# Kernel tuning notes

Measured on AMD Instinct MI355X. Metric: run time of the kernel, lower is better.

The kernel has to match this reference:

```python
import jax, jax.numpy as jnp
import numpy as np

TWO_PI = 2.0 * np.pi


def _fftfreq(n, d):
    # numpy-compatible fftfreq, trace/grad-safe in d: [0..n/2-1, -n/2..-1]/(n*d)
    k = jnp.arange(n)
    k = jnp.where(k < (n + 1) // 2, k, k - n).astype(jnp.float32)
    return k / (n * d)


def _forward(x, wp1_re, wp1_im, wp2_re, wp2_im, wr_re, wr_im, ty, tx):
    wp1 = (wp1_re + 1j * wp1_im).astype(jnp.complex64)   # [Ci,Co,m1]
    wp2 = (wp2_re + 1j * wp2_im).astype(jnp.complex64)   # [Ci,Co,m2]
    wr = (wr_re + 1j * wr_im).astype(jnp.complex64)      # [Ci,Co,m1,m2]
    Ny, Nx = x.shape[-2], x.shape[-1]
    dty = ty[1] - ty[0]
    dtx = tx[1] - tx[0]

    alpha = jnp.fft.fft2(x, axes=(-2, -1))               # [B,Ci,Ny,Nx] complex
    lam1 = (1j * TWO_PI * _fftfreq(Ny, dty)).astype(jnp.complex64)  # [Ny]
    lam2 = (1j * TWO_PI * _fftfreq(Nx, dtx)).astype(jnp.complex64)  # [Nx]

    # Pole-residue transfer function factors: Hw = wr / ((lam1-p1)(lam2-p2))
    A1 = 1.0 / (lam1 - wp1[..., None])                   # [Ci,Co,m1,Ny]
    A2 = 1.0 / (lam2 - wp2[..., None])                   # [Ci,Co,m2,Nx]

    # sum over poles (p,q) of Hw -> [Ci,Co,Ny,Nx]
    Hsum = jnp.einsum('ikpq,ikpo,ikqx->ikox', wr, A1, A2)
    res1 = jnp.einsum('biox,ikox->bkox', alpha, Hsum)    # [B,Co,Ny,Nx]
    # sum over frequency grid (o,x) -> residue coefficients [B,Co,m1,m2]
    res2 = jnp.einsum('biox,ikpq,ikpo,ikqx->bkpq', alpha, wr, A1, A2)

    x1 = jnp.real(jnp.fft.ifft2(res1, s=(Ny, Nx), axes=(-2, -1)))

    # explicit pole-exponential evaluation over the spatial grid
    E1 = jnp.exp(wp1[..., None] * ty.astype(jnp.complex64))  # [Ci,Co,m1,Ny]
    E2 = jnp.exp(wp2[..., None] * tx.astype(jnp.complex64))  # [Ci,Co,m2,Nx]
    # res2 channel dim contracts against E1/E2's first (in==out required)
    x2 = jnp.real(jnp.einsum('kbpq,bipz,biqx->kizx', res2, E1, E2)) / (Nx * Ny)
    return x1 + x2


def setup_inputs() -> dict:
    key = jax.random.key(0)
    B, Ci, Co, Ny, Nx, m1, m2 = 8, 32, 32, 128, 128, 4, 5
    ks = jax.random.split(key, 7)
    scale = 1.0 / (Ci * Co)
    x = jax.random.normal(ks[0], (B, Ci, Ny, Nx), jnp.float32)
    wp1_re = scale * jax.random.uniform(ks[1], (Ci, Co, m1), jnp.float32)
    wp1_im = scale * jax.random.uniform(ks[2], (Ci, Co, m1), jnp.float32)
    wp2_re = scale * jax.random.uniform(ks[3], (Ci, Co, m2), jnp.float32)
    wp2_im = scale * jax.random.uniform(ks[4], (Ci, Co, m2), jnp.float32)
    wr_re = scale * jax.random.uniform(ks[5], (Ci, Co, m1, m2), jnp.float32)
    wr_im = scale * jax.random.uniform(ks[6], (Ci, Co, m1, m2), jnp.float32)
    ty = (jnp.arange(Ny) / Ny).astype(jnp.float32)
    tx = (jnp.arange(Nx) / Nx).astype(jnp.float32)
    return dict(x=x, wp1_re=wp1_re, wp1_im=wp1_im, wp2_re=wp2_re, wp2_im=wp2_im,
                wr_re=wr_re, wr_im=wr_im, ty=ty, tx=tx)


def reference(x, wp1_re, wp1_im, wp2_re, wp2_im, wr_re, wr_im, ty, tx):
    return _forward(x, wp1_re, wp1_im, wp2_re, wp2_im, wr_re, wr_im, ty, tx)
```

## Files before the change

### kernel.cpp

```cpp
#include <hip/hip_runtime.h>
#include <math.h>

#define N 128
#define B 8
#define CI 32
#define CO 32
#define M1 4
#define M2 5
#define IK (CI*CO)
#define IKP (IK*M1)
#define IKQ (IK*M2)
#define TWO_PI_F 6.2831853071795864769f

__device__ __forceinline__ float2 cmul(float2 a, float2 b){
    return make_float2(fmaf(a.x,b.x,-(a.y*b.y)), fmaf(a.x,b.y,a.y*b.x));
}
__device__ __forceinline__ float2 cmadd(float2 acc, float2 a, float2 b){
    acc.x = fmaf(a.x, b.x, fmaf(-a.y, b.y, acc.x));
    acc.y = fmaf(a.x, b.y, fmaf( a.y, b.x, acc.y));
    return acc;
}

__global__ void k_A1T(const float* wr_, const float* wi_, const float* t_, float2* A1T){
    int idx = blockIdx.x*256 + threadIdx.x;
    int o   = idx >> 12;
    int ikp = idx & (IKP-1);
    float d = t_[1]-t_[0];
    float invnd = 1.0f/((float)N*d);
    int kk = (o < N/2) ? o : o - N;
    float lam = TWO_PI_F * (float)kk * invnd;
    float dr = -wr_[ikp];
    float di = lam - wi_[ikp];
    float inv = 1.0f/(dr*dr + di*di);
    A1T[idx] = make_float2(dr*inv, -di*inv);
}

__global__ void k_A2(const float* wr_, const float* wi_, const float* t_, float2* A2){
    int idx = blockIdx.x*256 + threadIdx.x;
    int ikq = idx >> 7; int xx = idx & (N-1);
    float d = t_[1]-t_[0];
    float invnd = 1.0f/((float)N*d);
    int kk = (xx < N/2) ? xx : xx - N;
    float lam = TWO_PI_F * (float)kk * invnd;
    float dr = -wr_[ikq];
    float di = lam - wi_[ikq];
    float inv = 1.0f/(dr*dr + di*di);
    A2[idx] = make_float2(dr*inv, -di*inv);
}

__global__ void k_E(const float* wr_, const float* wi_, const float* t_, float2* E){
    int idx = blockIdx.x*256 + threadIdx.x;
    int ikp = idx >> 7; int y = idx & (N-1);
    float t = t_[y];
    float m = expf(wr_[ikp]*t);
    float s, c; sincosf(wi_[ikp]*t, &s, &c);
    E[idx] = make_float2(m*c, m*s);
}

__global__ void k_W2N(const float* wrr, const float* wri, const float2* A2, float2* W2N){
    int idx = blockIdx.x*256 + threadIdx.x;
    int ikp = idx >> 7; int xx = idx & (N-1);
    int ik = ikp >> 2; int p = ikp & 3;
    float2 acc = make_float2(0.f,0.f);
    const float* wr0 = wrr + ik*(M1*M2) + p*M2;
    const float* wi0 = wri + ik*(M1*M2) + p*M2;
    const float2* a2 = A2 + (size_t)ik*(M2*N) + xx;
    #pragma unroll
    for(int q=0;q<M2;q++){
        float2 w = make_float2(wr0[q], wi0[q]);
        acc = cmadd(acc, w, a2[q*N]);
    }
    W2N[(size_t)ikp*N + xx] = acc;
}

template<int SIGNPOS, int REALIN, int SCALE>
__global__ void __launch_bounds__(256) k_fft_rows(const void* in_, float2* out){
    const float sgn = SIGNPOS ? 1.0f : -1.0f;
    __shared__ float tre[16*132];
    __shared__ float tim_[16*132];
    __shared__ float zre[16*136];
    __shared__ float zim[16*136];
    int t = threadIdx.x;
    size_t row0 = (size_t)blockIdx.x * 16;

    if(REALIN){
        const float* src = (const float*)in_ + row0*N;
        #pragma unroll
        for(int j=0;j<8;j++){
            int idx = t + 256*j; int r = idx>>7, cl = idx&127;
            tre[r*132+cl] = src[idx];
        }
    } else {
        const float2* src = (const float2*)in_ + row0*N;
        #pragma unroll
        for(int j=0;j<8;j++){
            int idx = t + 256*j; int r = idx>>7, cl = idx&127;
            float2 v = src[idx];
            tre[r*132+cl] = v.x; tim_[r*132+cl] = v.y;
        }
    }
    float t16c[16], t16s[16];
    #pragma unroll
    for(int j=0;j<16;j++){ float s,c; sincosf(sgn*(TWO_PI_F/16.f)*(float)j, &s,&c); t16c[j]=c; t16s[j]=s; }
    __syncthreads();

    int r = t>>4, u = t&15, b = u&7, h = u>>3;
    float xr[16], xi[16];
    #pragma unroll
    for(int a=0;a<16;a++){
        float vr = tre[r*132 + 8*a + b];
        float vi = REALIN ? 0.f : tim_[r*132 + 8*a + b];
        if(h && (a&1)){ vr = -vr; vi = -vi; }
        xr[a]=vr; xi[a]=vi;
    }
    #pragma unroll
    for(int cc=0; cc<8; cc++){
        float yr=0.f, yi=0.f;
        #pragma unroll
        for(int a=0;a<16;a++){
            int j = (a*cc)&15;
            if(REALIN){
                yr = fmaf(xr[a], t16c[j], yr);
                yi = fmaf(xr[a], t16s[j], yi);
            } else {
                yr = fmaf(xr[a], t16c[j], yr); yr = fmaf(-xi[a], t16s[j], yr);
                yi = fmaf(xr[a], t16s[j], yi); yi = fmaf( xi[a], t16c[j], yi);
            }
        }
        int c = 8*h + cc;
        float s,co; sincosf(sgn*(TWO_PI_F/128.f)*(float)(b*c), &s,&co);
        zre[r*136 + b*17 + c] = fmaf(yr,co,-(yi*s));
        zim[r*136 + b*17 + c] = fmaf(yr,s,  yi*co);
    }
    __syncthreads();

    float t8c[8], t8s[8];
    #pragma unroll
    for(int j=0;j<8;j++){ float s,c; sincosf(sgn*(TWO_PI_F/8.f)*(float)j, &s,&c); t8c[j]=c; t8s[j]=s; }
    int r2 = t>>4, c2 = t&15;
    float zr_[8], zi_[8];
    #pragma unroll
    for(int bb=0;bb<8;bb++){ zr_[bb]=zre[r2*136 + bb*17 + c2]; zi_[bb]=zim[r2*136 + bb*17 + c2]; }
    float2* dst = out + (row0 + r2)*N;
    #pragma unroll
    for(int d=0; d<8; d++){
        float Xr=0.f, Xi=0.f;
        #pragma unroll
        for(int bb=0;bb<8;bb++){
            int j=(bb*d)&7;
            Xr = fmaf(zr_[bb], t8c[j], Xr); Xr = fmaf(-zi_[bb], t8s[j], Xr);
            Xi = fmaf(zr_[bb], t8s[j], Xi); Xi = fmaf( zi_[bb], t8c[j], Xi);
        }
        if(SCALE){ Xr *= (1.f/128.f); Xi *= (1.f/128.f); }
        dst[c2 + 16*d] = make_float2(Xr, Xi);
    }
}

template<int SIGNPOS, int REALOUT, int SCALE>
__global__ void __launch_bounds__(256) k_fft_cols(const float2* in, float2* outc, float* outr){
    const float sgn = SIGNPOS ? 1.0f : -1.0f;
    __shared__ float tre[N*17];
    __shared__ float tim_[N*17];
    __shared__ float zre[8*16*17];
    __shared__ float zim[8*16*17];
    int t = threadIdx.x;
    int img = blockIdx.x >> 3; int x0 = (blockIdx.x & 7)*16;
    const float2* src = in + (size_t)img*N*N + x0;
    #pragma unroll
    for(int j=0;j<8;j++){
        int idx = t + 256*j; int y = idx>>4, xc = idx&15;
        float2 v = src[y*N + xc];
        tre[y*17+xc]=v.x; tim_[y*17+xc]=v.y;
    }
    float t16c[16], t16s[16];
    #pragma unroll
    for(int j=0;j<16;j++){ float s,c; sincosf(sgn*(TWO_PI_F/16.f)*(float)j, &s,&c); t16c[j]=c; t16s[j]=s; }
    __syncthreads();

    int xc = t&15, u = t>>4, b = u&7, h = u>>3;
    float xr[16], xi[16];
    #pragma unroll
    for(int a=0;a<16;a++){
        int y = 8*a + b;
        float vr = tre[y*17+xc];
        float vi = tim_[y*17+xc];
        if(h && (a&1)){ vr = -vr; vi = -vi; }
        xr[a]=vr; xi[a]=vi;
    }
    #pragma unroll
    for(int cc=0; cc<8; cc++){
        float yr=0.f, yi=0.f;
        #pragma unroll
        for(int a=0;a<16;a++){
            int j = (a*cc)&15;
            yr = fmaf(xr[a], t16c[j], yr); yr = fmaf(-xi[a], t16s[j], yr);
            yi = fmaf(xr[a], t16s[j], yi); yi = fmaf( xi[a], t16c[j], yi);
        }
        int c = 8*h + cc;
        float s,co; sincosf(sgn*(TWO_PI_F/128.f)*(float)(b*c), &s,&co);
        zre[(b*16 + c)*17 + xc] = fmaf(yr,co,-(yi*s));
        zim[(b*16 + c)*17 + xc] = fmaf(yr,s,  yi*co);
    }
    __syncthreads();

    float t8c[8], t8s[8];
    #pragma unroll
    for(int j=0;j<8;j++){ float s,c; sincosf(sgn*(TWO_PI_F/8.f)*(float)j, &s,&c); t8c[j]=c; t8s[j]=s; }
    int c2 = t>>4; int x2 = t&15;
    float zr_[8], zi_[8];
    #pragma unroll
    for(int bb=0;bb<8;bb++){ zr_[bb]=zre[(bb*16 + c2)*17 + x2]; zi_[bb]=zim[(bb*16 + c2)*17 + x2]; }
    #pragma unroll
    for(int d=0; d<8; d++){
        float Xr=0.f, Xi=0.f;
        #pragma unroll
        for(int bb=0;bb<8;bb++){
            int j=(bb*d)&7;
            Xr = fmaf(zr_[bb], t8c[j], Xr); Xr = fmaf(-zi_[bb], t8s[j], Xr);
            Xi = fmaf(zr_[bb], t8s[j], Xi); Xi = fmaf( zi_[bb], t8c[j], Xi);
        }
        int ky = c2 + 16*d;
        if(REALOUT){
            outr[(size_t)img*N*N + ky*N + x0 + x2] = Xr * (SCALE ? (1.f/128.f) : 1.f);
        } else {
            if(SCALE){ Xr *= (1.f/128.f); Xi *= (1.f/128.f); }
            outc[(size_t)img*N*N + ky*N + x0 + x2] = make_float2(Xr, Xi);
        }
    }
}

__global__ void __launch_bounds__(256) k_res1(const float2* alpha, const float2* A1T,
                                              const float2* W2N, float2* res1){
    __shared__ float4 At4[B*CI*8];
    int t = threadIdx.x;
    int o  = blockIdx.x >> 3;
    int x0 = (blockIdx.x & 7) * 16;

    {
        int im0 = t >> 3, xq = t & 7;
        #pragma unroll
        for(int j=0;j<8;j++){
            int im = im0 + 32*j;
            At4[im*8 + xq] = *(const float4*)(alpha + (size_t)im*(N*N) + o*N + x0 + 2*xq);
        }
    }
    __syncthreads();

    int k = t >> 3, xh = t & 7;
    float2 acc[B][2];
    #pragma unroll
    for(int b=0;b<B;b++){ acc[b][0]=make_float2(0.f,0.f); acc[b][1]=make_float2(0.f,0.f); }

    const float2* a1base = A1T + (size_t)o*IKP + k*M1;
    const float2* w2base = W2N + ((size_t)k*M1)*N + x0 + 2*xh;

    #pragma unroll 2
    for(int i=0;i<CI;i++){
        float4 a1a = *(const float4*)(a1base + (size_t)i*128);
        float4 a1b = *(const float4*)(a1base + (size_t)i*128 + 2);
        float2 a1v[M1] = { make_float2(a1a.x,a1a.y), make_float2(a1a.z,a1a.w),
                           make_float2(a1b.x,a1b.y), make_float2(a1b.z,a1b.w) };
        float2 h0 = make_float2(0.f,0.f), h1 = make_float2(0.f,0.f);
        const float2* w2 = w2base + (size_t)i*(128*N);
        #pragma unroll
        for(int p=0;p<M1;p++){
            float4 wv = *(const float4*)(w2 + (size_t)p*N);
            h0 = cmadd(h0, a1v[p], make_float2(wv.x,wv.y));
            h1 = cmadd(h1, a1v[p], make_float2(wv.z,wv.w));
        }
        #pragma unroll
        for(int b=0;b<B;b++){
            float4 av = At4[(b*CI + i)*8 + xh];
            acc[b][0] = cmadd(acc[b][0], make_float2(av.x,av.y), h0);
            acc[b][1] = cmadd(acc[b][1], make_float2(av.z,av.w), h1);
        }
    }

    #pragma unroll
    for(int b=0;b<B;b++){
        float4 v = make_float4(acc[b][0].x, acc[b][0].y, acc[b][1].x, acc[b][1].y);
        *(float4*)(res1 + (size_t)(b*CO + k)*(N*N) + o*N + x0 + 2*xh) = v;
    }
}

__global__ void __launch_bounds__(512) k_S_res2(const float2* alpha, const float2* A2,
                                                const float2* A1T, float2* part){
    __shared__ float2 tile[64*9];
    __shared__ float2 A2c[8*160];
    int t = threadIdx.x;
    int ol = t & 15;
    int kl = t >> 4;
    int bid = blockIdx.x;
    int oh = bid & 1;
    int i  = (bid >> 1) & (CI-1);
    int b  = bid >> 6;
    int ik = i*CO + kl;
    const float2* asrc = alpha + ((size_t)(b*CI + i))*(N*N) + (size_t)oh*64*N;

    const int trow = t >> 3, txc = t & 7;
    int a2dst[3]; size_t a2src[3]; bool a2ok[3];
    #pragma unroll
    for(int s=0;s<3;s++){
        int e = t + 512*s;
        a2ok[s] = (e < 1280);
        int e2 = a2ok[s] ? e : 0;
        int xcs = e2 / 160, rs = e2 - xcs*160;
        int kk = rs / 5, qq = rs - kk*5;
        a2dst[s] = e2;
        a2src[s] = ((size_t)(i*CO + kk)*M2 + qq)*N + xcs;
    }

    float2 U[4][5];
    #pragma unroll
    for(int oi=0;oi<4;oi++)
        #pragma unroll
        for(int q=0;q<5;q++) U[oi][q] = make_float2(0.f,0.f);

    float2 pre, a2pre[3];
    pre = asrc[trow*N + txc];
    #pragma unroll
    for(int s=0;s<3;s++) if(a2ok[s]) a2pre[s] = A2[a2src[s]];

    for(int c=0; c<16; c++){
        __syncthreads();
        tile[trow*9 + txc] = pre;
        #pragma unroll
        for(int s=0;s<3;s++) if(a2ok[s]) A2c[a2dst[s]] = a2pre[s];
        if(c < 15){
            int x0n = (c+1)*8;
            pre = asrc[trow*N + x0n + txc];
            #pragma unroll
            for(int s=0;s<3;s++) if(a2ok[s]) a2pre[s] = A2[a2src[s] + x0n];
        }
        __syncthreads();
        #pragma unroll
        for(int xc=0; xc<8; xc++){
            float2 a2v[5];
            const float2* a2row = A2c + xc*160 + kl*5;
            #pragma unroll
            for(int q=0;q<5;q++) a2v[q] = a2row[q];
            #pragma unroll
            for(int oi=0;oi<4;oi++){
                float2 av = tile[(ol + 16*oi)*9 + xc];
                #pragma unroll
                for(int q=0;q<5;q++) U[oi][q] = cmadd(U[oi][q], av, a2v[q]);
            }
        }
    }

    float2 S[4][5];
    #pragma unroll
    for(int p=0;p<4;p++)
        #pragma unroll
        for(int q=0;q<5;q++) S[p][q] = make_float2(0.f,0.f);
    #pragma unroll
    for(int oi=0;oi<4;oi++){
        int o = oh*64 + ol + 16*oi;
        const float2* a1 = A1T + (size_t)o*IKP + (size_t)ik*M1;
        float2 a1v[4];
        #pragma unroll
        for(int p=0;p<4;p++) a1v[p] = a1[p];
        #pragma unroll
        for(int p=0;p<4;p++)
            #pragma unroll
            for(int q=0;q<5;q++) S[p][q] = cmadd(S[p][q], a1v[p], U[oi][q]);
    }
    #pragma unroll
    for(int m=1;m<16;m<<=1){
        #pragma unroll
        for(int p=0;p<4;p++)
            #pragma unroll
            for(int q=0;q<5;q++){
                S[p][q].x += __shfl_xor(S[p][q].x, m);
                S[p][q].y += __shfl_xor(S[p][q].y, m);
            }
    }
    if(ol==0){
        float2* dst = part + ((size_t)((b*CO + kl)*CI + i)*2 + oh)*(M1*M2);
        #pragma unroll
        for(int p=0;p<4;p++)
            #pragma unroll
            for(int q=0;q<5;q++) dst[p*5+q] = S[p][q];
    }
}

__global__ void k_res2_red(const float2* part, const float* wrr, const float* wri, float2* res2){
    int bk = blockIdx.x;
    int t = threadIdx.x;
    int i = t & 31, g = t >> 5;
    int k = bk & (CO-1);
    int ikk = i*CO + k;
    float2 acc[5];
    #pragma unroll
    for(int e=0;e<5;e++){
        int pq = g*5 + e;
        float2 w = make_float2(wrr[ikk*(M1*M2)+pq], wri[ikk*(M1*M2)+pq]);
        const float2* pp = part + ((size_t)(bk*CI + i)*2)*(M1*M2) + pq;
        float2 s0 = pp[0], s1 = pp[M1*M2];
        float2 s = make_float2(s0.x+s1.x, s0.y+s1.y);
        acc[e] = cmul(w, s);
    }
    #pragma unroll
    for(int m=1;m<32;m<<=1){
        #pragma unroll
        for(int e=0;e<5;e++){
            acc[e].x += __shfl_xor(acc[e].x, m);
            acc[e].y += __shfl_xor(acc[e].y, m);
        }
    }
    if(i==0){
        #pragma unroll
        for(int e=0;e<5;e++) res2[(size_t)bk*(M1*M2) + g*5 + e] = acc[e];
    }
}

__global__ void __launch_bounds__(256) k_x2(const float2* res2, const float2* E1,
                                            const float2* E2, float* out){
    __shared__ __align__(16) float2 res2s[CI*M1*M2];
    __shared__ __align__(16) float2 Wt[M1*N];
    __shared__ __align__(16) float2 buf[2][M1*64 + M2*N];
    int t = threadIdx.x;
    int yh = blockIdx.x & 1;
    int j  = (blockIdx.x >> 1) & (CO-1);
    int b  = blockIdx.x >> 6;
    int xt = t & 15, yt = t >> 4;

    {
        const float4* s4 = (const float4*)(res2 + (size_t)b*CO*M1*M2);
        float4* d4 = (float4*)res2s;
        d4[t] = s4[t];
        if(t < 64) d4[256+t] = s4[256+t];
    }

    const bool is1_0 = (t < 128);
    const bool ok1 = (t < 192);
    int off0, dst0;
    if(is1_0){ int pp = t >> 5, rem = (t & 31) << 1; off0 = pp*N + rem; dst0 = pp*64 + rem; }
    else     { int g = t - 128; int qq = g >> 6, xi = (g & 63) << 1; off0 = qq*N + xi; dst0 = 256 + qq*128 + xi; }
    int g1 = t + 128; int qq1 = g1 >> 6, xi1 = (g1 & 63) << 1;
    int off1 = qq1*N + xi1;
    int dst1 = 256 + qq1*128 + xi1;

    const float2* E1c = E1 + ((size_t)j*M1)*N + yh*64;
    const float2* E2c = E2 + ((size_t)j*M2)*N;

    float4 pre0 = *(const float4*)((is1_0 ? E1c : E2c) + off0);
    float4 pre1 = ok1 ? *(const float4*)(E2c + off1) : make_float4(0.f,0.f,0.f,0.f);
    *(float4*)(&buf[0][dst0]) = pre0;
    if(ok1) *(float4*)(&buf[0][dst1]) = pre1;
    int cur = 0;
    __syncthreads();

    float acc[4][8];
    #pragma unroll
    for(int yy=0;yy<4;yy++)
        #pragma unroll
        for(int s=0;s<8;s++) acc[yy][s] = 0.f;

    for(int c=0; c<CI; c++){
        const float2* E2s = buf[cur] + 256;
        #pragma unroll
        for(int s=0;s<2;s++){
            int e = t + 256*s;
            int pp = e >> 7, xi = e & 127;
            const float2* rr = res2s + c*(M1*M2) + pp*M2;
            float2 w = make_float2(0.f,0.f);
            #pragma unroll
            for(int q=0;q<M2;q++) w = cmadd(w, rr[q], E2s[q*128 + xi]);
            Wt[pp*128 + xi] = w;
        }
        if(c+1 < CI){
            E1c += (size_t)CO*M1*N;
            E2c += (size_t)CO*M2*N;
            pre0 = *(const float4*)((is1_0 ? E1c : E2c) + off0);
            if(ok1) pre1 = *(const float4*)(E2c + off1);
        }
        __syncthreads();

        const float2* E1s = buf[cur];
        #pragma unroll
        for(int p=0;p<4;p++){
            float2 e1[4];
            float4 a  = *(const float4*)(E1s + p*64 + yt*4);
            float4 bq = *(const float4*)(E1s + p*64 + yt*4 + 2);
            e1[0]=make_float2(a.x,a.y);  e1[1]=make_float2(a.z,a.w);
            e1[2]=make_float2(bq.x,bq.y); e1[3]=make_float2(bq.z,bq.w);
            #pragma unroll
            for(int s=0;s<4;s++){
                float4 wv = *(const float4*)(Wt + p*128 + 32*s + 2*xt);
                #pragma unroll
                for(int yy=0;yy<4;yy++){
                    float2 e = e1[yy];
                    acc[yy][2*s]   = fmaf(e.x, wv.x, fmaf(-e.y, wv.y, acc[yy][2*s]));
                    acc[yy][2*s+1] = fmaf(e.x, wv.z, fmaf(-e.y, wv.w, acc[yy][2*s+1]));
                }
            }
        }
        if(c+1 < CI){
            float2* nb = buf[cur^1];
            *(float4*)(nb + dst0) = pre0;
            if(ok1) *(float4*)(nb + dst1) = pre1;
        }
        cur ^= 1;
        __syncthreads();
    }

    const float sc = 1.0f/((float)N*(float)N);
    size_t base = (size_t)(b*CO + j)*(N*N) + (size_t)yh*64*N;
    #pragma unroll
    for(int yy=0;yy<4;yy++){
        float* orow = out + base + (size_t)(yt*4 + yy)*N;
        #pragma unroll
        for(int s=0;s<4;s++){
            float2* dst = (float2*)(orow + 32*s + 2*xt);
            float2 old = *dst;
            *dst = make_float2(old.x + acc[yy][2*s]*sc, old.y + acc[yy][2*s+1]*sc);
        }
    }
}

extern "C" void kernel_launch(void* const* d_in, const int* in_sizes, int n_in,
                              void* d_out, int out_size, void* d_ws, size_t ws_size,
                              hipStream_t stream){
    const float* x    = (const float*)d_in[0];
    const float* wp1r = (const float*)d_in[1];
    const float* wp1i = (const float*)d_in[2];
    const float* wp2r = (const float*)d_in[3];
    const float* wp2i = (const float*)d_in[4];
    const float* wrr  = (const float*)d_in[5];
    const float* wri  = (const float*)d_in[6];
    const float* ty   = (const float*)d_in[7];
    const float* tx   = (const float*)d_in[8];
    float* out = (float*)d_out;
    float2* ws = (float2*)d_ws;

    const size_t NCIMG = (size_t)B*CI*N*N;
    float2* bufA  = ws;
    float2* alpha = bufA  + NCIMG;
    float2* res1  = alpha + NCIMG;
    float2* A1T   = res1  + NCIMG;
    float2* A2    = A1T   + (size_t)N*IKP;
    float2* W2N   = A2    + (size_t)IKQ*N;
    float2* E1    = W2N   + (size_t)N*IKP;
    float2* E2    = E1    + (size_t)IKP*N;
    float2* res2  = E2    + (size_t)IKQ*N;
    float2* part  = res2  + (size_t)B*CO*M1*M2;

    k_A1T<<<(N*IKP)/256, 256, 0, stream>>>(wp1r, wp1i, ty, A1T);
    k_E  <<<(IKP*N)/256, 256, 0, stream>>>(wp1r, wp1i, ty, E1);
    k_A2 <<<(IKQ*N)/256, 256, 0, stream>>>(wp2r, wp2i, tx, A2);
    k_E  <<<(IKQ*N)/256, 256, 0, stream>>>(wp2r, wp2i, tx, E2);
    k_W2N<<<(IKP*N)/256, 256, 0, stream>>>(wrr, wri, A2, W2N);

    k_fft_rows<0,1,0><<<(B*CI*N)/16, 256, 0, stream>>>((const void*)x, bufA);
    k_fft_cols<0,0,0><<<B*CI*8, 256, 0, stream>>>(bufA, alpha, nullptr);

    k_res1<<<N*8, 256, 0, stream>>>(alpha, A1T, W2N, res1);
    k_S_res2<<<B*CI*2, 512, 0, stream>>>(alpha, A2, A1T, part);
    k_res2_red<<<B*CO, 128, 0, stream>>>(part, wrr, wri, res2);

    k_fft_rows<1,0,1><<<(B*CO*N)/16, 256, 0, stream>>>((const void*)res1, bufA);
    k_fft_cols<1,1,1><<<B*CO*8, 256, 0, stream>>>(bufA, nullptr, out);
    k_x2<<<B*CO*2, 256, 0, stream>>>(res2, E1, E2, out);
}
```

Before: 314.6 us.

## Widen res2 x-chunk to 32 columns and coalesce A2 staging loads

Restructures the k_S_res2 staging loop to process 32 x-columns per chunk instead of 8, cutting the number of barrier-separated iterations from 16 to 4. A2 is now loaded with contiguous 32-wide rows (coalesced along x) into a padded transposed shared layout, instead of strided per-element gathers. Shared memory grows substantially (about 60KB per block), and a launch_bounds minimum-blocks hint is added; this may limit occupancy and forces A2 to be loaded synchronously without prefetch.

```diff
diff --git a/kernel.cpp b/kernel.cpp
--- a/kernel.cpp
+++ b/kernel.cpp
@@ -283,10 +283,10 @@
     }
 }
 
-__global__ void __launch_bounds__(512) k_S_res2(const float2* alpha, const float2* A2,
-                                                const float2* A1T, float2* part){
-    __shared__ float2 tile[64*9];
-    __shared__ float2 A2c[8*160];
+__global__ void __launch_bounds__(512, 4) k_S_res2(const float2* alpha, const float2* A2,
+                                                   const float2* A1T, float2* part){
+    __shared__ float2 tile[64*33];
+    __shared__ float2 A2c[160*33];
     int t = threadIdx.x;
     int ol = t & 15;
     int kl = t >> 4;
@@ -296,52 +296,42 @@
     int b  = bid >> 6;
     int ik = i*CO + kl;
     const float2* asrc = alpha + ((size_t)(b*CI + i))*(N*N) + (size_t)oh*64*N;
-
-    const int trow = t >> 3, txc = t & 7;
-    int a2dst[3]; size_t a2src[3]; bool a2ok[3];
-    #pragma unroll
-    for(int s=0;s<3;s++){
-        int e = t + 512*s;
-        a2ok[s] = (e < 1280);
-        int e2 = a2ok[s] ? e : 0;
-        int xcs = e2 / 160, rs = e2 - xcs*160;
-        int kk = rs / 5, qq = rs - kk*5;
-        a2dst[s] = e2;
-        a2src[s] = ((size_t)(i*CO + kk)*M2 + qq)*N + xcs;
-    }
-
+    const float2* a2base = A2 + (size_t)i*(CO*M2*N);
+
+    const int txc = t & 31, trow = t >> 5;
     float2 U[4][5];
     #pragma unroll
     for(int oi=0;oi<4;oi++)
         #pragma unroll
         for(int q=0;q<5;q++) U[oi][q] = make_float2(0.f,0.f);
 
-    float2 pre, a2pre[3];
-    pre = asrc[trow*N + txc];
-    #pragma unroll
-    for(int s=0;s<3;s++) if(a2ok[s]) a2pre[s] = A2[a2src[s]];
-
-    for(int c=0; c<16; c++){
+    float2 pre[4];
+    #pragma unroll
+    for(int j=0;j<4;j++) pre[j] = asrc[(trow + 16*j)*N + txc];
+
+    for(int c=0; c<4; c++){
         __syncthreads();
-        tile[trow*9 + txc] = pre;
-        #pragma unroll
-        for(int s=0;s<3;s++) if(a2ok[s]) A2c[a2dst[s]] = a2pre[s];
-        if(c < 15){
-            int x0n = (c+1)*8;
-            pre = asrc[trow*N + x0n + txc];
-            #pragma unroll
-            for(int s=0;s<3;s++) if(a2ok[s]) a2pre[s] = A2[a2src[s] + x0n];
+        #pragma unroll
+        for(int j=0;j<4;j++) tile[(trow + 16*j)*33 + txc] = pre[j];
+        #pragma unroll
+        for(int s=0;s<10;s++){
+            int rs = s*16 + trow;
+            A2c[rs*33 + txc] = a2base[(size_t)rs*N + c*32 + txc];
+        }
+        if(c < 3){
+            #pragma unroll
+            for(int j=0;j<4;j++) pre[j] = asrc[(trow + 16*j)*N + (c+1)*32 + txc];
         }
         __syncthreads();
-        #pragma unroll
-        for(int xc=0; xc<8; xc++){
+        #pragma unroll 4
+        for(int xc=0; xc<32; xc++){
             float2 a2v[5];
-            const float2* a2row = A2c + xc*160 + kl*5;
-            #pragma unroll
-            for(int q=0;q<5;q++) a2v[q] = a2row[q];
+            const float2* a2row = A2c + (kl*5)*33 + xc;
+            #pragma unroll
+            for(int q=0;q<5;q++) a2v[q] = a2row[q*33];
             #pragma unroll
             for(int oi=0;oi<4;oi++){
-                float2 av = tile[(ol + 16*oi)*9 + xc];
+                float2 av = tile[(ol + 16*oi)*33 + xc];
                 #pragma unroll
                 for(int q=0;q<5;q++) U[oi][q] = cmadd(U[oi][q], av, a2v[q]);
             }
```

Result: no change. 310.4 us (-1.3%).
